# Kernel tuning notes

Hardware: AMD Instinct MI355X
Metric: run time of the kernel (lower is better)

## Reference

```python
import jax, jax.numpy as jnp
import numpy as np

N, E = 50000, 800000
HID, HEADS, EDIM = 64, 4, 3
NEG_SLOPE = 0.2
LN_EPS = 1e-5


def setup_inputs() -> dict:
    key = jax.random.key(0)
    ks = jax.random.split(key, 12)
    h = jax.random.normal(ks[0], (N, HID), dtype=jnp.float32)
    edge_index = jax.random.randint(ks[1], (2, E), 0, N, dtype=jnp.int64)
    edge_attr = jax.random.normal(ks[2], (E, EDIM), dtype=jnp.float32)
    t = jax.random.uniform(ks[3], (1,), dtype=jnp.float32)
    s = 1.0 / np.sqrt(HID)
    W = jax.random.normal(ks[4], (HID, HEADS * HID), dtype=jnp.float32) * s
    att_src = jax.random.normal(ks[5], (1, HEADS, HID), dtype=jnp.float32) * s
    att_dst = jax.random.normal(ks[6], (1, HEADS, HID), dtype=jnp.float32) * s
    W_edge = jax.random.normal(ks[7], (EDIM, HEADS * HID), dtype=jnp.float32) * s
    att_edge = jax.random.normal(ks[8], (1, HEADS, HID), dtype=jnp.float32) * s
    bias = jnp.zeros((HID,), dtype=jnp.float32)
    ln_gamma = jnp.ones((HID,), dtype=jnp.float32)
    ln_beta = jnp.zeros((HID,), dtype=jnp.float32)
    return {"t": t, "h": h, "edge_index": edge_index, "edge_attr": edge_attr,
            "W": W, "att_src": att_src, "att_dst": att_dst, "W_edge": W_edge,
            "att_edge": att_edge, "bias": bias, "ln_gamma": ln_gamma, "ln_beta": ln_beta}


def reference(t, h, edge_index, edge_attr, W, att_src, att_dst, W_edge, att_edge, bias, ln_gamma, ln_beta):
    # GATConv (PyG, edge_dim>0, add_self_loops=False, concat=False, eval mode)
    x = (h @ W).reshape(N, HEADS, HID)                     # [N,H,C]
    a_src = (x * att_src).sum(-1)                          # [N,H]
    a_dst = (x * att_dst).sum(-1)                          # [N,H]
    e = (edge_attr @ W_edge).reshape(E, HEADS, HID)        # [E,H,C]
    a_edge = (e * att_edge).sum(-1)                        # [E,H]
    src, dst = edge_index[0], edge_index[1]
    alpha = a_src[src] + a_dst[dst] + a_edge               # [E,H]
    alpha = jax.nn.leaky_relu(alpha, NEG_SLOPE)
    # softmax over edges sharing the same destination node
    amax = jax.ops.segment_max(alpha, dst, num_segments=N)  # [N,H]
    ex = jnp.exp(alpha - amax[dst])
    esum = jax.ops.segment_sum(ex, dst, num_segments=N)     # [N,H]
    alpha = ex / (esum[dst] + 1e-16)
    msg = x[src] * alpha[:, :, None]                        # [E,H,C]
    out = jax.ops.segment_sum(msg, dst, num_segments=N)     # [N,H,C]
    out = out.mean(axis=1) + bias                           # concat=False -> head mean
    # LayerNorm + SiLU
    mu = out.mean(-1, keepdims=True)
    var = ((out - mu) ** 2).mean(-1, keepdims=True)
    y = (out - mu) * jax.lax.rsqrt(var + LN_EPS) * ln_gamma + ln_beta
    return y * jax.nn.sigmoid(y)
```

## Files before the change

### kernel.cpp

```cpp
#include <hip/hip_runtime.h>
#include <hip/hip_bf16.h>

#define HIDC 64
#define NEG_SLOPE 0.2f
#define SCAN_G 128

typedef __hip_bfloat16 bf16;
typedef short bf16x8 __attribute__((ext_vector_type(8)));
typedef float floatx4 __attribute__((ext_vector_type(4)));
typedef int intx4 __attribute__((ext_vector_type(4)));

static __device__ __forceinline__ float b2f(bf16 v) { return __bfloat162float(v); }

static __device__ __forceinline__ unsigned short f2us(float f) {
  bf16 b = __float2bfloat16(f);
  union { bf16 b; unsigned short u; } c;
  c.b = b;
  return c.u;
}

template <bool FF>
static __device__ __forceinline__ float ld(const void* __restrict__ p, size_t i) {
  return FF ? ((const float*)p)[i] : b2f(((const bf16*)p)[i]);
}
static __device__ __forceinline__ float ldr(const void* __restrict__ p, size_t i,
                                            bool ff) {
  return ff ? ((const float*)p)[i] : b2f(((const bf16*)p)[i]);
}
template <bool I64>
static __device__ __forceinline__ int ldi(const int* __restrict__ p, long long i) {
  return I64 ? (int)((const long long*)p)[i] : p[i];
}
static __device__ __forceinline__ int clampN(int v, int N) {
  return ((unsigned)v < (unsigned)N) ? v : 0;
}

static __device__ __forceinline__ int4 ntload4(const int4* __restrict__ p) {
  intx4 v = __builtin_nontemporal_load((const intx4*)p);
  return make_int4(v.x, v.y, v.z, v.w);
}

static __device__ __forceinline__ bool det_f32(const unsigned* __restrict__ hw) {
  unsigned w = hw[threadIdx.x & 31];
  int ex = (w >> 7) & 0xFF;
  unsigned long long b = __ballot(ex >= 99 && ex <= 135);
  return __popcll(b) < 32;
}
static __device__ __forceinline__ bool det_i64(const int* __restrict__ ei) {
  int v = ei[2 * (threadIdx.x & 31) + 1];
  return __ballot(v != 0) == 0ULL;
}

template <bool FF, bool I64>
static __device__ __forceinline__ void xh_body(
    const void* __restrict__ h, const void* __restrict__ W,
    const void* __restrict__ att_src, const void* __restrict__ att_dst,
    const int* __restrict__ ei, bf16* __restrict__ x,
    float* __restrict__ a_src, float* __restrict__ a_dst,
    int* __restrict__ cnt, int N, int E,
    unsigned short* __restrict__ hls, unsigned short* __restrict__ wls) {
  for (long long e = (long long)blockIdx.x * 256 + threadIdx.x; e < E;
       e += (long long)gridDim.x * 256) {
    int dst = clampN(ldi<I64>(ei, (long long)E + e), N);
    atomicAdd(&cnt[dst], 1);
  }
  const int t = threadIdx.x;
  const long long n0 = (long long)blockIdx.x * 64;
  {
    const int c = t;
    const int jn = c & 63, hd = c >> 6;
    const int r = hd * 64 + (jn & 3) * 16 + (jn >> 2);
#pragma unroll
    for (int q = 0; q < 8; q++) {
      unsigned short u[8];
#pragma unroll
      for (int j = 0; j < 8; j++) {
        int k = q * 8 + j;
        u[j] = FF ? f2us(((const float*)W)[(size_t)k * 256 + c])
                  : ((const unsigned short*)W)[(size_t)k * 256 + c];
      }
      int4 v = make_int4((int)(u[0] | ((unsigned)u[1] << 16)),
                         (int)(u[2] | ((unsigned)u[3] << 16)),
                         (int)(u[4] | ((unsigned)u[5] << 16)),
                         (int)(u[6] | ((unsigned)u[7] << 16)));
      *(int4*)&wls[r * 64 + (q ^ (r & 7)) * 8] = v;
    }
  }
  {
    const int row = t >> 2;
    const long long n = n0 + row;
#pragma unroll
    for (int dq = 0; dq < 2; dq++) {
      int q = (t & 3) * 2 + dq;
      int4 v;
      if (n < N) {
        if (FF) {
          const float4* hp = (const float4*)h + n * 16 + q * 2;
          float4 f0 = hp[0], f1 = hp[1];
          v = make_int4((int)(f2us(f0.x) | ((unsigned)f2us(f0.y) << 16)),
                        (int)(f2us(f0.z) | ((unsigned)f2us(f0.w) << 16)),
                        (int)(f2us(f1.x) | ((unsigned)f2us(f1.y) << 16)),
                        (int)(f2us(f1.z) | ((unsigned)f2us(f1.w) << 16)));
        } else {
          v = *((const int4*)((const unsigned short*)h + n * 64 + q * 8));
        }
      } else {
        v = make_int4(0, 0, 0, 0);
      }
      *(int4*)&hls[row * 64 + (q ^ (row & 7)) * 8] = v;
    }
  }
  __syncthreads();
  const int w = t >> 6;
  const int lane = t & 63;
  const int lm = lane & 15, lq = lane >> 4;
  bf16x8 af[4][2];
#pragma unroll
  for (int nt = 0; nt < 4; nt++)
#pragma unroll
    for (int ks = 0; ks < 2; ks++) {
      int m = nt * 16 + lm;
      int q = ks * 4 + lq;
      af[nt][ks] = *(const bf16x8*)&hls[m * 64 + (q ^ (m & 7)) * 8];
    }
  floatx4 acc[4][4];
#pragma unroll
  for (int nt = 0; nt < 4; nt++)
#pragma unroll
    for (int ct = 0; ct < 4; ct++) acc[nt][ct] = (floatx4){0.f, 0.f, 0.f, 0.f};
#pragma unroll
  for (int ct = 0; ct < 4; ct++) {
    int c = w * 64 + ct * 16 + lm;
    bf16x8 b0 = *(const bf16x8*)&wls[c * 64 + ((lq) ^ (c & 7)) * 8];
    bf16x8 b1 = *(const bf16x8*)&wls[c * 64 + ((4 + lq) ^ (c & 7)) * 8];
#pragma unroll
    for (int nt = 0; nt < 4; nt++) {
      acc[nt][ct] = __builtin_amdgcn_mfma_f32_16x16x32_bf16(af[nt][0], b0,
                                                            acc[nt][ct], 0, 0, 0);
      acc[nt][ct] = __builtin_amdgcn_mfma_f32_16x16x32_bf16(af[nt][1], b1,
                                                            acc[nt][ct], 0, 0, 0);
    }
  }
  float as_c[4], ad_c[4];
#pragma unroll
  for (int ct = 0; ct < 4; ct++) {
    as_c[ct] = ld<FF>(att_src, w * 64 + lm * 4 + ct);
    ad_c[ct] = ld<FF>(att_dst, w * 64 + lm * 4 + ct);
  }
#pragma unroll
  for (int nt = 0; nt < 4; nt++) {
    float ps[4] = {0.f, 0.f, 0.f, 0.f}, pd[4] = {0.f, 0.f, 0.f, 0.f};
#pragma unroll
    for (int ct = 0; ct < 4; ct++) {
#pragma unroll
      for (int r = 0; r < 4; r++) {
        ps[r] += acc[nt][ct][r] * as_c[ct];
        pd[r] += acc[nt][ct][r] * ad_c[ct];
      }
    }
    long long nb = n0 + nt * 16 + lq * 4;
#pragma unroll
    for (int r = 0; r < 4; r++) {
      long long n = nb + r;
      if (n < N) {
        ushort4 us = make_ushort4(f2us(acc[nt][0][r]), f2us(acc[nt][1][r]),
                                  f2us(acc[nt][2][r]), f2us(acc[nt][3][r]));
        *(ushort4*)&x[n * 256 + w * 64 + lm * 4] = us;
      }
    }
#pragma unroll
    for (int mask = 1; mask < 16; mask <<= 1) {
#pragma unroll
      for (int r = 0; r < 4; r++) {
        ps[r] += __shfl_xor(ps[r], mask);
        pd[r] += __shfl_xor(pd[r], mask);
      }
    }
    if (lm == 0) {
#pragma unroll
      for (int r = 0; r < 4; r++) {
        long long n = nb + r;
        if (n < N) {
          a_src[n * 4 + w] = ps[r];
          a_dst[n * 4 + w] = pd[r];
        }
      }
    }
  }
}

__global__ void __launch_bounds__(256) k_xh(
    const void* __restrict__ h, const void* __restrict__ W,
    const void* __restrict__ att_src, const void* __restrict__ att_dst,
    const int* __restrict__ ei, bf16* __restrict__ x,
    float* __restrict__ a_src, float* __restrict__ a_dst,
    int* __restrict__ cnt, int N, int E) {
  __shared__ alignas(16) unsigned short hls[64 * 64];
  __shared__ alignas(16) unsigned short wls[256 * 64];
  bool f32 = det_f32((const unsigned*)h);
  bool i64 = det_i64(ei);
  if (f32) {
    if (i64) xh_body<true, true>(h, W, att_src, att_dst, ei, x, a_src, a_dst, cnt, N, E, hls, wls);
    else     xh_body<true, false>(h, W, att_src, att_dst, ei, x, a_src, a_dst, cnt, N, E, hls, wls);
  } else {
    if (i64) xh_body<false, true>(h, W, att_src, att_dst, ei, x, a_src, a_dst, cnt, N, E, hls, wls);
    else     xh_body<false, false>(h, W, att_src, att_dst, ei, x, a_src, a_dst, cnt, N, E, hls, wls);
  }
}

__global__ void __launch_bounds__(1024) k_bscan(
    const void* __restrict__ W_edge, const void* __restrict__ att_edge,
    const unsigned* __restrict__ hw, const int* __restrict__ cnt,
    int* __restrict__ offs, int* __restrict__ bsum, int* __restrict__ bbase,
    int* __restrict__ done, float* __restrict__ M, int N) {
  int b = blockIdx.x, t = threadIdx.x;
  if (b == 0 && t < 768) {
    bool ff = det_f32(hw);
    int wv = t >> 6, lane = t & 63;
    int d = wv >> 2, hh = wv & 3;
    float p = ldr(W_edge, (size_t)d * 256 + hh * 64 + lane, ff) *
              ldr(att_edge, (size_t)hh * 64 + lane, ff);
#pragma unroll
    for (int o = 32; o; o >>= 1) p += __shfl_down(p, o);
    if (lane == 0) M[d * 4 + hh] = p;
  }
  const int C = (N + SCAN_G - 1) / SCAN_G;
  const int b0 = b * C;
  __shared__ int ts[1024];
  __shared__ int lastf;
  int v = 0;
  if (t < C && b0 + t < N) v = cnt[b0 + t];
  ts[t] = v;
  __syncthreads();
  for (int off = 1; off < 1024; off <<= 1) {
    int u = (t >= off) ? ts[t - off] : 0;
    __syncthreads();
    ts[t] += u;
    __syncthreads();
  }
  if (t < C && b0 + t < N) offs[b0 + t] = ts[t] - v;
  if (t == 1023) {
    atomicExch(&bsum[b], ts[1023]);
    __threadfence();
    int old = atomicAdd(done, 1);
    lastf = (old == SCAN_G - 1) ? 1 : 0;
  }
  __syncthreads();
  if (lastf) {
    int w = (t < SCAN_G) ? atomicAdd(&bsum[t], 0) : 0;
    ts[t] = w;
    __syncthreads();
    for (int off = 1; off < 1024; off <<= 1) {
      int u = (t >= off) ? ts[t - off] : 0;
      __syncthreads();
      ts[t] += u;
      __syncthreads();
    }
    if (t < SCAN_G) bbase[t] = ts[t] - w;
  }
}

__global__ void __launch_bounds__(1024) k_add(
    int* __restrict__ offs, int* __restrict__ cursor,
    const int* __restrict__ bbase, int N, int E) {
  int b = blockIdx.x, t = threadIdx.x;
  const int C = (N + SCAN_G - 1) / SCAN_G;
  const int b0 = b * C;
  int base = bbase[b];
  if (t < C && b0 + t < N) {
    int o = offs[b0 + t] + base;
    offs[b0 + t] = o;
    cursor[b0 + t] = o;
  }
  if (b == 0 && t == 0) offs[N] = E;
}

template <bool FF, bool I64>
static __device__ __forceinline__ void es_body(
    const int* __restrict__ ei, const void* __restrict__ eattr,
    const float* __restrict__ a_src, const float* __restrict__ a_dst,
    const float* __restrict__ M, int* __restrict__ cursor,
    int4* __restrict__ slots, int E, int N, unsigned* __restrict__ sattr) {
  const long long e0 = (long long)blockIdx.x * 256;
  {
    const unsigned bpe = FF ? 12u : 6u;
    const unsigned* gsrc = (const unsigned*)((const char*)eattr + e0 * bpe);
    unsigned ndw = FF ? 768u : 384u;
    long long bytes_left = ((long long)E - e0) * bpe;
    if (bytes_left < 0) bytes_left = 0;
    unsigned max_dw = (unsigned)((bytes_left + 3) >> 2);
    if (ndw > max_dw) ndw = max_dw;
    for (unsigned i = threadIdx.x; i < ndw; i += 256) sattr[i] = gsrc[i];
  }
  __syncthreads();
  long long e = e0 + threadIdx.x;
  if (e >= E) return;
  int src = clampN(ldi<I64>(ei, e), N);
  int dst = clampN(ldi<I64>(ei, (long long)E + e), N);
  float ea0, ea1, ea2;
  if (FF) {
    const float* sf = (const float*)sattr;
    ea0 = sf[threadIdx.x * 3 + 0];
    ea1 = sf[threadIdx.x * 3 + 1];
    ea2 = sf[threadIdx.x * 3 + 2];
  } else {
    const unsigned short* su = (const unsigned short*)sattr;
    ea0 = __uint_as_float((unsigned)su[threadIdx.x * 3 + 0] << 16);
    ea1 = __uint_as_float((unsigned)su[threadIdx.x * 3 + 1] << 16);
    ea2 = __uint_as_float((unsigned)su[threadIdx.x * 3 + 2] << 16);
  }
  const float4 m0 = ((const float4*)M)[0];
  const float4 m1 = ((const float4*)M)[1];
  const float4 m2 = ((const float4*)M)[2];
  const float4 as4 = ((const float4*)a_src)[src];
  const float4 ad4 = ((const float4*)a_dst)[dst];
  float al[4];
  al[0] = as4.x + ad4.x + ea0 * m0.x + ea1 * m1.x + ea2 * m2.x;
  al[1] = as4.y + ad4.y + ea0 * m0.y + ea1 * m1.y + ea2 * m2.y;
  al[2] = as4.z + ad4.z + ea0 * m0.z + ea1 * m1.z + ea2 * m2.z;
  al[3] = as4.w + ad4.w + ea0 * m0.w + ea1 * m1.w + ea2 * m2.w;
  unsigned short u[4];
#pragma unroll
  for (int hh = 0; hh < 4; hh++) {
    float a = al[hh];
    a = (a > 0.f) ? a : NEG_SLOPE * a;
    a = fminf(fmaxf(a, -60.f), 60.f);
    u[hh] = f2us(__expf(a));
  }
  int pos = atomicAdd(&cursor[dst], 1);
  slots[pos] = make_int4(src, (int)(u[0] | ((unsigned)u[1] << 16)),
                         (int)(u[2] | ((unsigned)u[3] << 16)), 0);
}

__global__ void __launch_bounds__(256) k_es(
    const int* __restrict__ ei, const void* __restrict__ eattr,
    const float* __restrict__ a_src, const float* __restrict__ a_dst,
    const float* __restrict__ M, const unsigned* __restrict__ hw,
    int* __restrict__ cursor, int4* __restrict__ slots, int E, int N) {
  __shared__ unsigned sattr[768];
  bool f32 = det_f32(hw);
  bool i64 = det_i64(ei);
  if (f32) {
    if (i64) es_body<true, true>(ei, eattr, a_src, a_dst, M, cursor, slots, E, N, sattr);
    else     es_body<true, false>(ei, eattr, a_src, a_dst, M, cursor, slots, E, N, sattr);
  } else {
    if (i64) es_body<false, true>(ei, eattr, a_src, a_dst, M, cursor, slots, E, N, sattr);
    else     es_body<false, false>(ei, eattr, a_src, a_dst, M, cursor, slots, E, N, sattr);
  }
}

static __device__ __forceinline__ uint2 xgat(const uint2* __restrict__ xr,
                                             int src, int lane) {
  int ss = __builtin_amdgcn_readfirstlane(src);
  return xr[(size_t)(unsigned)ss * 64 + lane];
}

__global__ void __launch_bounds__(256) k_agg(
    const int* __restrict__ offs, const int4* __restrict__ slots,
    const unsigned* __restrict__ xu, const unsigned* __restrict__ hw,
    const void* __restrict__ bias, const void* __restrict__ gamma,
    const void* __restrict__ beta, void* __restrict__ out, int N) {
  const int t = threadIdx.x;
  const int wv = t >> 6, lane = t & 63;
  const int n = blockIdx.x * 4 + wv;
  if (n >= N) return;
  const int head2 = lane >> 5;
  const unsigned wshift = (lane & 16) ? 0u : 16u;
  const uint2* __restrict__ xr = (const uint2*)xu;

  int s0 = __builtin_amdgcn_readfirstlane(offs[n]);
  int s1 = __builtin_amdgcn_readfirstlane(offs[n + 1]);

  float a0 = 0.f, a1 = 0.f, a2 = 0.f, a3 = 0.f, ws = 0.f;

#define ACC4(q, d)                                                    \
  do {                                                                \
    unsigned ee = head2 ? (unsigned)(q).z : (unsigned)(q).y;          \
    float wv_ = __uint_as_float((ee << wshift) & 0xffff0000u);        \
    a0 += wv_ * __uint_as_float((d).x << 16);                         \
    a1 += wv_ * __uint_as_float((d).x & 0xffff0000u);                 \
    a2 += wv_ * __uint_as_float((d).y << 16);                         \
    a3 += wv_ * __uint_as_float((d).y & 0xffff0000u);                 \
    ws += wv_;                                                        \
  } while (0)

  int i = s0;
  for (; i + 8 <= s1; i += 8) {
    int4 q0 = ntload4(&slots[i + 0]);
    int4 q1 = ntload4(&slots[i + 1]);
    int4 q2 = ntload4(&slots[i + 2]);
    int4 q3 = ntload4(&slots[i + 3]);
    int4 q4 = ntload4(&slots[i + 4]);
    int4 q5 = ntload4(&slots[i + 5]);
    int4 q6 = ntload4(&slots[i + 6]);
    int4 q7 = ntload4(&slots[i + 7]);
    uint2 d0 = xgat(xr, q0.x, lane);
    uint2 d1 = xgat(xr, q1.x, lane);
    uint2 d2 = xgat(xr, q2.x, lane);
    uint2 d3 = xgat(xr, q3.x, lane);
    uint2 d4 = xgat(xr, q4.x, lane);
    uint2 d5 = xgat(xr, q5.x, lane);
    uint2 d6 = xgat(xr, q6.x, lane);
    uint2 d7 = xgat(xr, q7.x, lane);
    ACC4(q0, d0); ACC4(q1, d1); ACC4(q2, d2); ACC4(q3, d3);
    ACC4(q4, d4); ACC4(q5, d5); ACC4(q6, d6); ACC4(q7, d7);
  }
  for (; i + 4 <= s1; i += 4) {
    int4 q0 = ntload4(&slots[i + 0]);
    int4 q1 = ntload4(&slots[i + 1]);
    int4 q2 = ntload4(&slots[i + 2]);
    int4 q3 = ntload4(&slots[i + 3]);
    uint2 d0 = xgat(xr, q0.x, lane);
    uint2 d1 = xgat(xr, q1.x, lane);
    uint2 d2 = xgat(xr, q2.x, lane);
    uint2 d3 = xgat(xr, q3.x, lane);
    ACC4(q0, d0); ACC4(q1, d1); ACC4(q2, d2); ACC4(q3, d3);
  }
  for (; i < s1; i++) {
    int4 q = ntload4(&slots[i]);
    uint2 d = xgat(xr, q.x, lane);
    ACC4(q, d);
  }
#undef ACC4

  float inv = 1.f / (ws + 1e-16f);
  float v0 = a0 * inv, v1 = a1 * inv, v2 = a2 * inv, v3 = a3 * inv;
  v0 += __shfl_xor(v0, 16); v1 += __shfl_xor(v1, 16);
  v2 += __shfl_xor(v2, 16); v3 += __shfl_xor(v3, 16);
  v0 += __shfl_xor(v0, 32); v1 += __shfl_xor(v1, 32);
  v2 += __shfl_xor(v2, 32); v3 += __shfl_xor(v3, 32);

  bool ff = det_f32(hw);
  const int c0 = (lane & 15) * 4;
  float m0 = v0 * 0.25f + ldr(bias, c0 + 0, ff);
  float m1 = v1 * 0.25f + ldr(bias, c0 + 1, ff);
  float m2 = v2 * 0.25f + ldr(bias, c0 + 2, ff);
  float m3 = v3 * 0.25f + ldr(bias, c0 + 3, ff);

  float s = (m0 + m1) + (m2 + m3);
  s += __shfl_xor(s, 1); s += __shfl_xor(s, 2);
  s += __shfl_xor(s, 4); s += __shfl_xor(s, 8);
  float mu = s * 0.015625f;
  float d0 = m0 - mu, d1 = m1 - mu, d2 = m2 - mu, d3 = m3 - mu;
  float vq = (d0 * d0 + d1 * d1) + (d2 * d2 + d3 * d3);
  vq += __shfl_xor(vq, 1); vq += __shfl_xor(vq, 2);
  vq += __shfl_xor(vq, 4); vq += __shfl_xor(vq, 8);
  float rstd = rsqrtf(vq * 0.015625f + 1e-5f);

  if ((lane >> 4) == 0) {
    float y0 = d0 * rstd * ldr(gamma, c0 + 0, ff) + ldr(beta, c0 + 0, ff);
    float y1 = d1 * rstd * ldr(gamma, c0 + 1, ff) + ldr(beta, c0 + 1, ff);
    float y2 = d2 * rstd * ldr(gamma, c0 + 2, ff) + ldr(beta, c0 + 2, ff);
    float y3 = d3 * rstd * ldr(gamma, c0 + 3, ff) + ldr(beta, c0 + 3, ff);
    float r0 = y0 / (1.f + __expf(-y0));
    float r1 = y1 / (1.f + __expf(-y1));
    float r2 = y2 / (1.f + __expf(-y2));
    float r3 = y3 / (1.f + __expf(-y3));
    size_t ob = (size_t)n * 64 + c0;
    if (ff) {
      *(float4*)((float*)out + ob) = make_float4(r0, r1, r2, r3);
    } else {
      *(ushort4*)((bf16*)out + ob) =
          make_ushort4(f2us(r0), f2us(r1), f2us(r2), f2us(r3));
    }
  }
}

extern "C" void kernel_launch(void* const* d_in, const int* in_sizes, int n_in,
                              void* d_out, int out_size, void* d_ws,
                              size_t ws_size, hipStream_t stream) {
  const void* h        = d_in[1];
  const int*  ei       = (const int*)d_in[2];
  const void* eattr    = d_in[3];
  const void* W        = d_in[4];
  const void* att_src  = d_in[5];
  const void* att_dst  = d_in[6];
  const void* W_edge   = d_in[7];
  const void* att_edge = d_in[8];
  const void* bias     = d_in[9];
  const void* gamma    = d_in[10];
  const void* beta     = d_in[11];

  const int N = in_sizes[1] / HIDC;
  const int E = in_sizes[3] / 3;

  char* p = (char*)d_ws;
  float* M    = (float*)p; p += 64;
  bf16* x     = (bf16*)p;  p += (size_t)N * 256 * 2;
  float* asrc = (float*)p; p += (size_t)N * 4 * 4;
  float* adst = (float*)p; p += (size_t)N * 4 * 4;
  int4* slots = (int4*)p;  p += (size_t)E * 16;
  int* cnt    = (int*)p;   p += (size_t)N * 4;
  int* done   = (int*)p;   p += 64;
  int* offs   = (int*)p;   p += ((size_t)N + 4) * 4;
  int* cursor = (int*)p;   p += (size_t)N * 4;
  int* bsum   = (int*)p;   p += SCAN_G * 4;
  int* bbase  = (int*)p;   p += SCAN_G * 4;

  size_t need = (size_t)(p - (char*)d_ws);
  if (ws_size < need || N <= 0 || E <= 0) {
    hipMemsetAsync(d_out, 0, (size_t)out_size * 2, stream);
    return;
  }

  hipMemsetAsync(cnt, 0, (size_t)N * 4 + 64, stream);

  k_xh<<<(N + 63) / 64, 256, 0, stream>>>(h, W, att_src, att_dst, ei, x,
                                          asrc, adst, cnt, N, E);
  k_bscan<<<SCAN_G, 1024, 0, stream>>>(W_edge, att_edge, (const unsigned*)h,
                                       cnt, offs, bsum, bbase, done, M, N);
  k_add<<<SCAN_G, 1024, 0, stream>>>(offs, cursor, bbase, N, E);
  k_es<<<(E + 255) / 256, 256, 0, stream>>>(ei, eattr, asrc, adst, M,
                                            (const unsigned*)h, cursor, slots,
                                            E, N);
  k_agg<<<(N + 3) / 4, 256, 0, stream>>>(offs, slots, (const unsigned*)x,
                                         (const unsigned*)h, bias, gamma, beta,
                                         d_out, N);
}
```

Measured before the change: 261.1 us.

## Split aggregation into column-sliced gather kernel plus LayerNorm finalize kernel

Replaces the single per-node aggregation kernel with two passes. The first launches 8 blocks per group of nodes, each covering a 32-byte column slice of x for one head, processing 8 edges at a time across lane groups and writing normalized bf16 partials. The second sums the head partials and applies bias, LayerNorm and SiLU. Slot writes and reads become nontemporal. The goal is more parallelism and better cache locality in the gather, at the cost of an extra launch, a partial buffer round trip, reloading the edge slots 8 times, and a dependence on having enough workspace.

```diff
diff --git a/kernel.cpp b/kernel.cpp
--- a/kernel.cpp
+++ b/kernel.cpp
@@ -9,6 +9,7 @@
 typedef short bf16x8 __attribute__((ext_vector_type(8)));
 typedef float floatx4 __attribute__((ext_vector_type(4)));
 typedef int intx4 __attribute__((ext_vector_type(4)));
+typedef unsigned uintx2 __attribute__((ext_vector_type(2)));
 
 static __device__ __forceinline__ float b2f(bf16 v) { return __bfloat162float(v); }
 
@@ -18,6 +19,12 @@
   c.b = b;
   return c.u;
 }
+static __device__ __forceinline__ float blo(unsigned u) {
+  return __uint_as_float(u << 16);
+}
+static __device__ __forceinline__ float bhi(unsigned u) {
+  return __uint_as_float(u & 0xffff0000u);
+}
 
 template <bool FF>
 static __device__ __forceinline__ float ld(const void* __restrict__ p, size_t i) {
@@ -38,6 +45,20 @@
 static __device__ __forceinline__ int4 ntload4(const int4* __restrict__ p) {
   intx4 v = __builtin_nontemporal_load((const intx4*)p);
   return make_int4(v.x, v.y, v.z, v.w);
+}
+static __device__ __forceinline__ void ntstore4(int4 v, int4* __restrict__ p) {
+  intx4 w;
+  w.x = v.x; w.y = v.y; w.z = v.z; w.w = v.w;
+  __builtin_nontemporal_store(w, (intx4*)p);
+}
+static __device__ __forceinline__ int ntload1(const int* __restrict__ p) {
+  return __builtin_nontemporal_load(p);
+}
+static __device__ __forceinline__ void ntstore2(unsigned x, unsigned y,
+                                                unsigned* __restrict__ p) {
+  uintx2 v;
+  v.x = x; v.y = y;
+  __builtin_nontemporal_store(v, (uintx2*)p);
 }
 
 static __device__ __forceinline__ bool det_f32(const unsigned* __restrict__ hw) {
@@ -328,8 +349,9 @@
     u[hh] = f2us(__expf(a));
   }
   int pos = atomicAdd(&cursor[dst], 1);
-  slots[pos] = make_int4(src, (int)(u[0] | ((unsigned)u[1] << 16)),
-                         (int)(u[2] | ((unsigned)u[3] << 16)), 0);
+  ntstore4(make_int4(src, (int)(u[0] | ((unsigned)u[1] << 16)),
+                     (int)(u[2] | ((unsigned)u[3] << 16)), 0),
+           &slots[pos]);
 }
 
 __global__ void __launch_bounds__(256) k_es(
@@ -346,6 +368,110 @@
   } else {
     if (i64) es_body<false, true>(ei, eattr, a_src, a_dst, M, cursor, slots, E, N, sattr);
     else     es_body<false, false>(ei, eattr, a_src, a_dst, M, cursor, slots, E, N, sattr);
+  }
+}
+
+__global__ void __launch_bounds__(256) k_slice(
+    const int* __restrict__ offs, const int* __restrict__ sw,
+    const unsigned* __restrict__ xu, unsigned* __restrict__ part, int N) {
+  const int t = threadIdx.x;
+  const int wv = t >> 6, lane = t & 63;
+  const int b = blockIdx.x;
+  const int s = b & 7;
+  const int n = (b >> 3) * 4 + wv;
+  if (n >= N) return;
+  const int hs = s >> 1;
+  const int wsel = (hs < 2) ? 1 : 2;
+  const unsigned wshift = (hs & 1) ? 0u : 16u;
+  const int g = lane >> 3;
+  const int sub = lane & 7;
+  const uint2* __restrict__ xr2 = (const uint2*)xu;
+
+  int s0 = __builtin_amdgcn_readfirstlane(offs[n]);
+  int s1 = __builtin_amdgcn_readfirstlane(offs[n + 1]);
+
+  float a0 = 0.f, a1 = 0.f, a2 = 0.f, a3 = 0.f, ws = 0.f;
+#pragma unroll 2
+  for (int i = s0; i < s1; i += 8) {
+    int idx = i + g;
+    bool valid = idx < s1;
+    int idxc = valid ? idx : s0;
+    int src = ntload1(&sw[idxc * 4]);
+    unsigned wwd = (unsigned)ntload1(&sw[idxc * 4 + wsel]);
+    uint2 d = xr2[(size_t)(unsigned)src * 64 + (unsigned)(s * 8 + sub)];
+    float w = valid ? __uint_as_float((wwd << wshift) & 0xffff0000u) : 0.f;
+    a0 += w * blo(d.x);
+    a1 += w * bhi(d.x);
+    a2 += w * blo(d.y);
+    a3 += w * bhi(d.y);
+    ws += w;
+  }
+  a0 += __shfl_xor(a0, 8);  a1 += __shfl_xor(a1, 8);
+  a2 += __shfl_xor(a2, 8);  a3 += __shfl_xor(a3, 8);
+  ws += __shfl_xor(ws, 8);
+  a0 += __shfl_xor(a0, 16); a1 += __shfl_xor(a1, 16);
+  a2 += __shfl_xor(a2, 16); a3 += __shfl_xor(a3, 16);
+  ws += __shfl_xor(ws, 16);
+  a0 += __shfl_xor(a0, 32); a1 += __shfl_xor(a1, 32);
+  a2 += __shfl_xor(a2, 32); a3 += __shfl_xor(a3, 32);
+  ws += __shfl_xor(ws, 32);
+
+  if (lane < 8) {
+    float inv = 1.f / (ws + 1e-16f);
+    unsigned px = (unsigned)f2us(a0 * inv) | ((unsigned)f2us(a1 * inv) << 16);
+    unsigned py = (unsigned)f2us(a2 * inv) | ((unsigned)f2us(a3 * inv) << 16);
+    ntstore2(px, py, part + ((size_t)n * 128 + (size_t)(s * 8 + lane) * 2));
+  }
+}
+
+__global__ void __launch_bounds__(256) k_fin(
+    const unsigned* __restrict__ part, const unsigned* __restrict__ hw,
+    const void* __restrict__ bias, const void* __restrict__ gamma,
+    const void* __restrict__ beta, void* __restrict__ out, int N) {
+  const int t = threadIdx.x;
+  const int wv = t >> 6, lane = t & 63;
+  const int n = blockIdx.x * 4 + wv;
+  if (n >= N) return;
+  uint2 d = ((const uint2*)part)[(size_t)n * 64 + lane];
+  float v0 = blo(d.x), v1 = bhi(d.x), v2 = blo(d.y), v3 = bhi(d.y);
+  v0 += __shfl_xor(v0, 16); v1 += __shfl_xor(v1, 16);
+  v2 += __shfl_xor(v2, 16); v3 += __shfl_xor(v3, 16);
+  v0 += __shfl_xor(v0, 32); v1 += __shfl_xor(v1, 32);
+  v2 += __shfl_xor(v2, 32); v3 += __shfl_xor(v3, 32);
+
+  bool ff = det_f32(hw);
+  const int c0 = (lane & 15) * 4;
+  float m0 = v0 * 0.25f + ldr(bias, c0 + 0, ff);
+  float m1 = v1 * 0.25f + ldr(bias, c0 + 1, ff);
+  float m2 = v2 * 0.25f + ldr(bias, c0 + 2, ff);
+  float m3 = v3 * 0.25f + ldr(bias, c0 + 3, ff);
+
+  float s = (m0 + m1) + (m2 + m3);
+  s += __shfl_xor(s, 1); s += __shfl_xor(s, 2);
+  s += __shfl_xor(s, 4); s += __shfl_xor(s, 8);
+  float mu = s * 0.015625f;
+  float d0 = m0 - mu, d1 = m1 - mu, d2 = m2 - mu, d3 = m3 - mu;
+  float vq = (d0 * d0 + d1 * d1) + (d2 * d2 + d3 * d3);
+  vq += __shfl_xor(vq, 1); vq += __shfl_xor(vq, 2);
+  vq += __shfl_xor(vq, 4); vq += __shfl_xor(vq, 8);
+  float rstd = rsqrtf(vq * 0.015625f + 1e-5f);
+
+  if ((lane >> 4) == 0) {
+    float y0 = d0 * rstd * ldr(gamma, c0 + 0, ff) + ldr(beta, c0 + 0, ff);
+    float y1 = d1 * rstd * ldr(gamma, c0 + 1, ff) + ldr(beta, c0 + 1, ff);
+    float y2 = d2 * rstd * ldr(gamma, c0 + 2, ff) + ldr(beta, c0 + 2, ff);
+    float y3 = d3 * rstd * ldr(gamma, c0 + 3, ff) + ldr(beta, c0 + 3, ff);
+    float r0 = y0 / (1.f + __expf(-y0));
+    float r1 = y1 / (1.f + __expf(-y1));
+    float r2 = y2 / (1.f + __expf(-y2));
+    float r3 = y3 / (1.f + __expf(-y3));
+    size_t ob = (size_t)n * 64 + c0;
+    if (ff) {
+      *(float4*)((float*)out + ob) = make_float4(r0, r1, r2, r3);
+    } else {
+      *(ushort4*)((bf16*)out + ob) =
+          make_ushort4(f2us(r0), f2us(r1), f2us(r2), f2us(r3));
+    }
   }
 }
 
@@ -498,10 +624,14 @@
   int* bbase  = (int*)p;   p += SCAN_G * 4;
 
   size_t need = (size_t)(p - (char*)d_ws);
+  unsigned* part = (unsigned*)p;
+  size_t need2 = need + (size_t)N * 256 * 2;
+
   if (ws_size < need || N <= 0 || E <= 0) {
     hipMemsetAsync(d_out, 0, (size_t)out_size * 2, stream);
     return;
   }
+  const bool sliced = (ws_size >= need2);
 
   hipMemsetAsync(cnt, 0, (size_t)N * 4 + 64, stream);
 
@@ -513,7 +643,14 @@
   k_es<<<(E + 255) / 256, 256, 0, stream>>>(ei, eattr, asrc, adst, M,
                                             (const unsigned*)h, cursor, slots,
                                             E, N);
-  k_agg<<<(N + 3) / 4, 256, 0, stream>>>(offs, slots, (const unsigned*)x,
-                                         (const unsigned*)h, bias, gamma, beta,
-                                         d_out, N);
-}
+  if (sliced) {
+    k_slice<<<8 * ((N + 3) / 4), 256, 0, stream>>>(offs, (const int*)slots,
+                                                   (const unsigned*)x, part, N);
+    k_fin<<<(N + 3) / 4, 256, 0, stream>>>(part, (const unsigned*)h, bias,
+                                           gamma, beta, d_out, N);
+  } else {
+    k_agg<<<(N + 3) / 4, 256, 0, stream>>>(offs, slots, (const unsigned*)x,
+                                           (const unsigned*)h, bias, gamma,
+                                           beta, d_out, N);
+  }
+}
```

Result: slower. 403.3 us (+54.4%).
